# Kernel tuning notes

Hardware: AMD Instinct MI355X
Metric: run time of the kernel (lower is better)

The kernel has to match this reference:

```python
import math
import jax, jax.numpy as jnp
import numpy as np

TOP_K, NC, ALPHA, BETA, EPS = 10, 80, 0.5, 6.0, 1e-9
IMG, STRIDES = 640, (8, 16, 32)


def _ciou(box1, box2, eps=1e-7):
    # box1: gt [bs,n,1,4], box2: pred [bs,1,na,4] -> [bs,n,na,1]
    b1x1, b1y1, b1x2, b1y2 = jnp.split(box1, 4, axis=-1)
    b2x1, b2y1, b2x2, b2y2 = jnp.split(box2, 4, axis=-1)
    w1, h1 = b1x2 - b1x1, b1y2 - b1y1 + eps
    w2, h2 = b2x2 - b2x1, b2y2 - b2y1 + eps
    inter = jnp.clip(jnp.minimum(b1x2, b2x2) - jnp.maximum(b1x1, b2x1), 0.0) * \
            jnp.clip(jnp.minimum(b1y2, b2y2) - jnp.maximum(b1y1, b2y1), 0.0)
    union = w1 * h1 + w2 * h2 - inter + eps
    iou = inter / union
    cw = jnp.maximum(b1x2, b2x2) - jnp.minimum(b1x1, b2x1)
    ch = jnp.maximum(b1y2, b2y2) - jnp.minimum(b1y1, b2y1)
    c2 = cw ** 2 + ch ** 2 + eps
    rho2 = ((b2x1 + b2x2 - b1x1 - b1x2) ** 2 + (b2y1 + b2y2 - b1y1 - b1y2) ** 2) / 4.0
    v = (4.0 / math.pi ** 2) * (jnp.arctan(w2 / h2) - jnp.arctan(w1 / h1)) ** 2
    alpha = jax.lax.stop_gradient(v / (v - iou + (1.0 + eps)))
    return iou - (rho2 / c2 + v * alpha)


def _assign(score, p_box, anchors, gt_labels, gt_box, mask):
    bs, na, nc = score.shape
    n = gt_box.shape[1]
    labels = gt_labels[..., 0].astype(jnp.int32)      # [bs,n]
    valid = mask > 0                                  # [bs,n,1] valid-gt mask
    # --- candidate mask: anchor center strictly inside gt box ---
    lt, rb = gt_box[..., :2], gt_box[..., 2:]
    d = jnp.concatenate([anchors[None, None] - lt[:, :, None],
                         rb[:, :, None] - anchors[None, None]], -1)  # [bs,n,na,4]
    mask_in_gts = d.min(-1) > 1e-9                    # [bs,n,na]
    mask_gts = mask_in_gts & valid
    # --- per-(gt,anchor) class score and CIoU overlap ---
    gathered = score[jnp.arange(bs)[:, None], :, labels]          # [bs,n,na]
    bbox_scores = jnp.where(mask_gts, gathered, 0.0)
    ov = _ciou(gt_box[:, :, None], p_box[:, None])[..., 0]        # [bs,n,na]
    overlaps = jnp.where(mask_gts, jnp.clip(ov, 0.0), 0.0)
    metric = jnp.where(mask_gts,
                       jnp.where(mask_gts, gathered, 1.0) ** ALPHA * overlaps ** BETA,
                       0.0)
    # --- top-k candidates per gt; suppress duplicated indices ---
    _, top_id = jax.lax.top_k(metric, TOP_K)          # [bs,n,TOP_K]
    top_id = jnp.where(valid, top_id, 0)
    bi = jnp.arange(bs)[:, None, None]
    ni = jnp.arange(n)[None, :, None]
    count = jnp.zeros((bs, n, na), jnp.int32).at[bi, ni, top_id].add(1)
    count = jnp.where(count > 1, 0, count)
    mask_pos = count.astype(metric.dtype) * mask_in_gts.astype(metric.dtype) * mask  # [bs,n,na]
    fg = mask_pos.sum(1)                              # [bs,na]
    # --- resolve anchors claimed by multiple gts via max overlap ---
    max_over = (jnp.arange(n)[None, :, None] == jnp.argmax(overlaps, 1)[:, None, :]).astype(metric.dtype)
    mask_pos = jnp.where(fg[:, None, :] > 1, max_over, mask_pos)
    fg = mask_pos.sum(1)
    # --- gather targets ---
    gt_idx = jnp.argmax(mask_pos, 1)                  # [bs,na]
    target_labels = jnp.clip(jnp.take_along_axis(labels, gt_idx, 1), 0)
    target_bboxes = jnp.take_along_axis(gt_box, gt_idx[..., None], 1)  # [bs,na,4]
    ts = jax.nn.one_hot(target_labels, NC, dtype=metric.dtype)
    ts = jnp.where(fg[..., None] > 0, ts, 0.0)
    # --- task-aligned score normalization ---
    metric = metric * mask_pos
    pos_metrics = metric.max(-1, keepdims=True)
    pos_overlaps = (overlaps * mask_pos).max(-1, keepdims=True)
    norm_metric = metric * pos_overlaps / (pos_metrics + EPS)
    target_scores = ts * norm_metric.max(1)[..., None]               # [bs,na,NC]
    return target_bboxes, target_scores, fg > 0


def setup_inputs() -> dict:
    key = jax.random.key(0)
    ks = jax.random.split(key, 8)
    bs, n_max = 16, 64
    # anchor points: grid cell centers for strides 8/16/32 at 640x640
    pts = []
    for s in STRIDES:
        g = IMG // s
        c = (jnp.arange(g, dtype=jnp.float32) + 0.5) * s
        gy, gx = jnp.meshgrid(c, c, indexing='ij')
        pts.append(jnp.stack([gx.ravel(), gy.ravel()], -1))
    anchors = jnp.concatenate(pts, 0)                 # [8400,2]
    na = anchors.shape[0]
    # predicted boxes centered near anchor points
    wh = jax.random.uniform(ks[0], (bs, na, 2), minval=8.0, maxval=128.0)
    ctr = anchors[None] + jax.random.normal(ks[1], (bs, na, 2)) * 4.0
    p_box = jnp.concatenate([ctr - wh / 2, ctr + wh / 2], -1)
    score = jax.random.uniform(ks[2], (bs, na, NC))
    # ground-truth boxes (valid x1<x2, y1<y2)
    gwh = jax.random.uniform(ks[3], (bs, n_max, 2), minval=16.0, maxval=256.0)
    gctr = jax.random.uniform(ks[4], (bs, n_max, 2), minval=0.0, maxval=float(IMG))
    gt_box = jnp.concatenate([gctr - gwh / 2, gctr + gwh / 2], -1)
    gt_labels = jax.random.randint(ks[5], (bs, n_max, 1), 0, NC)
    nvalid = jax.random.randint(ks[6], (bs, 1), 8, n_max + 1)
    mask = (jnp.arange(n_max)[None, :] < nvalid).astype(jnp.float32)[..., None]
    return {"score": score, "p_box": p_box, "anchors": anchors,
            "gt_labels": gt_labels, "gt_box": gt_box, "mask": mask}


def reference(score, p_box, anchors, gt_labels, gt_box, mask):
    return _assign(score, p_box, anchors, gt_labels, gt_box, mask)
```

## Files before the change

### kernel.cpp

```cpp
#include <hip/hip_runtime.h>
#include <math.h>

#define BS   16
#define NMAX 64
#define NA   8400
#define NCLS 80
#define TOPK 10
#define ROWS (BS * NMAX)
#define TOTAL (BS * NA)

typedef unsigned long long u64;

__device__ __forceinline__ float ciou_clip(
    float gx1, float gy1, float gx2, float gy2, float at1, float area1,
    float px1, float py1, float px2, float py2, float at2, float area2)
{
    float iw = fminf(gx2, px2) - fmaxf(gx1, px1);
    float ih = fminf(gy2, py2) - fmaxf(gy1, py1);
    float inter = fmaxf(iw, 0.f) * fmaxf(ih, 0.f);
    float uni = area1 + area2 - inter + 1e-7f;
    float iou = inter / uni;
    float cw = fmaxf(gx2, px2) - fminf(gx1, px1);
    float ch = fmaxf(gy2, py2) - fminf(gy1, py1);
    float c2 = cw * cw + ch * ch + 1e-7f;
    float dx = px1 + px2 - gx1 - gx2;
    float dy = py1 + py2 - gy1 - gy2;
    float rho2 = (dx * dx + dy * dy) * 0.25f;
    float dat = at2 - at1;
    float v = (4.0f / (float)(M_PI * M_PI)) * dat * dat;
    float alpha = v / (v - iou + (1.0f + 1e-7f));
    return fmaxf(iou - (rho2 / c2 + v * alpha), 0.f);
}

#define INS10(kk)                                                         \
    if ((kk) > L[9]) {                                                    \
        L[9] = (kk);                                                      \
        _Pragma("unroll")                                                 \
        for (int q = 9; q >= 1; q--)                                      \
            if (L[q] > L[q-1]) { u64 tt = L[q-1]; L[q-1] = L[q]; L[q] = tt; } \
    }

__global__ __launch_bounds__(128) void k1_rows(
    const float* __restrict__ score,
    const float* __restrict__ p_box,
    const int*   __restrict__ gt_labels,
    const float* __restrict__ gt_box,
    const float* __restrict__ mask,
    u64*   __restrict__ mask64,
    float* __restrict__ amt,
    float* __restrict__ aov)
{
    int row = blockIdx.x;
    if (mask[row] <= 0.f) return;
    int wid  = threadIdx.x >> 6;
    int lane = threadIdx.x & 63;
    int b = row >> 6, n = row & 63;

    float4 gb = ((const float4*)gt_box)[row];
    float w1 = gb.z - gb.x;
    float h1 = gb.w - gb.y + 1e-7f;
    float at1 = atanf(w1 / h1);
    float area1 = w1 * h1;
    int lbl = gt_labels[row];
    const float* sc = score + (size_t)b * NA * NCLS + lbl;
    const float4* pb = (const float4*)p_box + (size_t)b * NA;

    int ilo0 = max(0,  (int)floorf(gb.x * 0.125f   - 0.5f));
    int ihi0 = min(79, (int)ceilf (gb.z * 0.125f   - 0.5f));
    int jlo0 = max(0,  (int)floorf(gb.y * 0.125f   - 0.5f));
    int jhi0 = min(79, (int)ceilf (gb.w * 0.125f   - 0.5f));
    int ilo1 = max(0,  (int)floorf(gb.x * 0.0625f  - 0.5f));
    int ihi1 = min(39, (int)ceilf (gb.z * 0.0625f  - 0.5f));
    int jlo1 = max(0,  (int)floorf(gb.y * 0.0625f  - 0.5f));
    int jhi1 = min(39, (int)ceilf (gb.w * 0.0625f  - 0.5f));
    int ilo2 = max(0,  (int)floorf(gb.x * 0.03125f - 0.5f));
    int ihi2 = min(19, (int)ceilf (gb.z * 0.03125f - 0.5f));
    int jlo2 = max(0,  (int)floorf(gb.y * 0.03125f - 0.5f));
    int jhi2 = min(19, (int)ceilf (gb.w * 0.03125f - 0.5f));
    int nx0 = max(0, ihi0 - ilo0 + 1), ny0 = max(0, jhi0 - jlo0 + 1);
    int nx1 = max(0, ihi1 - ilo1 + 1), ny1 = max(0, jhi1 - jlo1 + 1);
    int nx2 = max(0, ihi2 - ilo2 + 1), ny2 = max(0, jhi2 - jlo2 + 1);
    int c0 = nx0 * ny0;
    int c1 = c0 + nx1 * ny1;
    int T  = c1 + nx2 * ny2;

    u64 L[10];
#pragma unroll
    for (int q = 0; q < 10; q++) L[q] = 0ull;

    for (int t = threadIdx.x; t < T; t += 128) {
        bool ge1 = t >= c0, ge2 = t >= c1;
        int local = t - (ge2 ? c1 : (ge1 ? c0 : 0));
        int nxl  = ge2 ? nx2  : (ge1 ? nx1  : nx0);
        int ilol = ge2 ? ilo2 : (ge1 ? ilo1 : ilo0);
        int jlol = ge2 ? jlo2 : (ge1 ? jlo1 : jlo0);
        int g    = ge2 ? 20   : (ge1 ? 40   : 80);
        int off  = ge2 ? 8000 : (ge1 ? 6400 : 0);
        float s  = ge2 ? 32.f : (ge1 ? 16.f : 8.f);
        int jj = local / nxl;
        int ii = local - jj * nxl;
        int i = ilol + ii, j = jlol + jj;
        int a = off + j * g + i;
        float ax = ((float)i + 0.5f) * s, ay = ((float)j + 0.5f) * s;
        float dmin = fminf(fminf(ax - gb.x, ay - gb.y),
                           fminf(gb.z - ax, gb.w - ay));
        if (dmin > 1e-9f) {
            float4 pv = pb[a];
            float w2 = pv.z - pv.x;
            float h2 = pv.w - pv.y + 1e-7f;
            float ov = ciou_clip(gb.x, gb.y, gb.z, gb.w, at1, area1,
                                 pv.x, pv.y, pv.z, pv.w,
                                 atanf(w2 / h2), w2 * h2);
            float o2 = ov * ov;
            float mt = sqrtf(sc[(size_t)a * NCLS]) * o2 * o2 * o2;
            u64 kk = ((u64)__float_as_uint(mt) << 32) | (unsigned)(~a);
            INS10(kk)
        }
    }
    if (wid == 0) {
        float ax = (float)lane * 8.f + 4.f, ay = 4.f;
        float dmin = fminf(fminf(ax - gb.x, ay - gb.y),
                           fminf(gb.z - ax, gb.w - ay));
        if (!(dmin > 1e-9f)) {
            u64 kk = (u64)(unsigned)(~lane);
            INS10(kk)
        }
    }

    __shared__ u64 skey[2 * TOPK];
    u64 wk = 0ull;
    for (int it = 0; it < TOPK; it++) {
        u64 m = L[0];
#pragma unroll
        for (int o = 1; o < 64; o <<= 1) {
            u64 v = __shfl_xor(m, o);
            if (v > m) m = v;
        }
        if (lane == it) wk = m;
        if (L[0] == m) {
#pragma unroll
            for (int q = 0; q < 9; q++) L[q] = L[q + 1];
            L[9] = 0ull;
        }
    }
    if (lane < TOPK) skey[wid * TOPK + lane] = wk;
    __syncthreads();

    if (wid == 0) {
        u64 ck = (lane < 2 * TOPK) ? skey[lane] : 0ull;
        u64 winkey = 0ull;
        for (int it = 0; it < TOPK; it++) {
            u64 m = ck;
#pragma unroll
            for (int o = 1; o < 64; o <<= 1) {
                u64 v = __shfl_xor(m, o);
                if (v > m) m = v;
            }
            if (lane == it) winkey = m;
            if (ck == m) ck = 0ull;
        }
        if (lane < TOPK && winkey) {
            int a = (int)(~(unsigned)(winkey & 0xffffffffu));
            float mt = __uint_as_float((unsigned)(winkey >> 32));
            bool l2a = a >= 8000, l1a = (a >= 6400) && !l2a;
            int loc = a - (l2a ? 8000 : (l1a ? 6400 : 0));
            int g   = l2a ? 20 : (l1a ? 40 : 80);
            float s = l2a ? 32.f : (l1a ? 16.f : 8.f);
            int j = loc / g, i = loc - j * g;
            float ax = ((float)i + 0.5f) * s, ay = ((float)j + 0.5f) * s;
            float dmin = fminf(fminf(ax - gb.x, ay - gb.y),
                               fminf(gb.z - ax, gb.w - ay));
            if (dmin > 1e-9f) {
                size_t idx = (size_t)b * NA + a;
                atomicOr(&mask64[idx], 1ull << n);
                float4 pv = pb[a];
                float w2 = pv.z - pv.x;
                float h2 = pv.w - pv.y + 1e-7f;
                float ov = ciou_clip(gb.x, gb.y, gb.z, gb.w, at1, area1,
                                     pv.x, pv.y, pv.z, pv.w,
                                     atanf(w2 / h2), w2 * h2);
                amt[idx] = mt;
                aov[idx] = ov;
            }
        }
    }
}

__global__ __launch_bounds__(256) void k3_resolve(
    const float* __restrict__ score,
    const float* __restrict__ p_box,
    const float* __restrict__ anchors,
    const int*   __restrict__ gt_labels,
    const float* __restrict__ gt_box,
    const float* __restrict__ mask,
    const u64*   __restrict__ mask64,
    const float* __restrict__ amt,
    const float* __restrict__ aov,
    int* __restrict__ gt_idx,
    unsigned char* __restrict__ fg_arr,
    float* __restrict__ tgt_mt,
    float* __restrict__ out_bbox,
    float* __restrict__ out_fg,
    float* __restrict__ pos_mt,
    float* __restrict__ pos_ov)
{
    int i = blockIdx.x * 256 + threadIdx.x;
    if (i >= TOTAL) return;
    int b = i / NA, a = i - b * NA;
    u64 bits = mask64[i];
    int fg0 = __popcll(bits);
    int gi = 0, fg = (fg0 > 0);
    float mt = 0.f, ov = 0.f;
    if (fg0 == 1) {
        gi = __ffsll(bits) - 1;
        mt = amt[i];
        ov = aov[i];
    } else if (fg0 > 1) {
        float2 axy = ((const float2*)anchors)[a];
        float4 pv = ((const float4*)p_box)[i];
        float w2 = pv.z - pv.x;
        float h2 = pv.w - pv.y + 1e-7f;
        float at2 = atanf(w2 / h2);
        float area2 = w2 * h2;
        const float* mrow = mask + b * NMAX;
        float best = -1.f; int argn = 0;
        for (int nn = 0; nn < NMAX; nn++) {
            float v = 0.f;
            if (mrow[nn] > 0.f) {
                int r = b * NMAX + nn;
                float4 gbv = ((const float4*)gt_box)[r];
                float dmin = fminf(fminf(axy.x - gbv.x, axy.y - gbv.y),
                                   fminf(gbv.z - axy.x, gbv.w - axy.y));
                if (dmin > 1e-9f) {
                    float w1 = gbv.z - gbv.x;
                    float h1 = gbv.w - gbv.y + 1e-7f;
                    v = ciou_clip(gbv.x, gbv.y, gbv.z, gbv.w,
                                  atanf(w1 / h1), w1 * h1,
                                  pv.x, pv.y, pv.z, pv.w, at2, area2);
                }
            }
            if (v > best) { best = v; argn = nn; }
        }
        gi = argn;
        ov = fmaxf(best, 0.f);
        int lbl = gt_labels[b * NMAX + argn]; if (lbl < 0) lbl = 0;
        float gath = score[((size_t)b * NA + a) * NCLS + lbl];
        float o2 = ov * ov;
        mt = sqrtf(gath) * o2 * o2 * o2;
    }
    int r = b * NMAX + gi;
    gt_idx[i] = gi;
    fg_arr[i] = (unsigned char)fg;
    tgt_mt[i] = mt;
    out_fg[i] = fg ? 1.f : 0.f;
    ((float4*)out_bbox)[i] = ((const float4*)gt_box)[r];
    if (fg) {
        atomicMax((int*)&pos_mt[r], __float_as_int(mt));
        atomicMax((int*)&pos_ov[r], __float_as_int(ov));
    }
}

__global__ __launch_bounds__(256) void k5_full(
    const int*   __restrict__ gt_idx,
    const unsigned char* __restrict__ fg_arr,
    const float* __restrict__ tgt_mt,
    const int*   __restrict__ gt_labels,
    const float* __restrict__ pos_mt,
    const float* __restrict__ pos_ov,
    float4* __restrict__ out_scores)
{
    int i = blockIdx.x * 256 + threadIdx.x;
    if (i >= TOTAL * (NCLS / 4)) return;
    int ba = i / (NCLS / 4);
    int c4 = (i - ba * (NCLS / 4)) * 4;
    float4 o = make_float4(0.f, 0.f, 0.f, 0.f);
    if (fg_arr[ba]) {
        int b = ba / NA;
        int r = b * NMAX + gt_idx[ba];
        int lbl = gt_labels[r]; if (lbl < 0) lbl = 0;
        if (lbl >= c4 && lbl < c4 + 4) {
            float val = tgt_mt[ba] * pos_ov[r] / (pos_mt[r] + 1e-9f);
            if (lbl == c4)     o.x = val;
            if (lbl == c4 + 1) o.y = val;
            if (lbl == c4 + 2) o.z = val;
            if (lbl == c4 + 3) o.w = val;
        }
    }
    out_scores[i] = o;
}

extern "C" void kernel_launch(void* const* d_in, const int* in_sizes, int n_in,
                              void* d_out, int out_size, void* d_ws, size_t ws_size,
                              hipStream_t stream) {
    (void)in_sizes; (void)n_in; (void)out_size; (void)ws_size;
    const float* score     = (const float*)d_in[0];
    const float* p_box     = (const float*)d_in[1];
    const float* anchors   = (const float*)d_in[2];
    const int*   gt_labels = (const int*)d_in[3];
    const float* gt_box    = (const float*)d_in[4];
    const float* mask      = (const float*)d_in[5];

    char* w = (char*)d_ws;
    u64*   mask64   = (u64*)w;                 w += (size_t)TOTAL * 8;
    float* pos_mt   = (float*)w;               w += (size_t)ROWS * 4;
    float* pos_ov   = (float*)w;               w += (size_t)ROWS * 4;
    float* amt      = (float*)w;               w += (size_t)TOTAL * 4;
    float* aov      = (float*)w;               w += (size_t)TOTAL * 4;
    int*   gt_idx   = (int*)w;                 w += (size_t)TOTAL * 4;
    float* tgt_mt   = (float*)w;               w += (size_t)TOTAL * 4;
    unsigned char* fg_arr = (unsigned char*)w; w += (size_t)TOTAL;

    float*  out_bbox   = (float*)d_out;
    float4* out_scores = (float4*)(out_bbox + (size_t)TOTAL * 4);
    float*  out_fg     = (float*)out_scores + (size_t)TOTAL * NCLS;

    hipMemsetAsync(mask64, 0, (size_t)TOTAL * 8 + (size_t)ROWS * 8, stream);

    hipLaunchKernelGGL(k1_rows, dim3(ROWS), dim3(128), 0, stream,
                       score, p_box, gt_labels, gt_box, mask,
                       mask64, amt, aov);
    hipLaunchKernelGGL(k3_resolve, dim3((TOTAL + 255) / 256), dim3(256), 0, stream,
                       score, p_box, anchors, gt_labels, gt_box, mask,
                       mask64, amt, aov,
                       gt_idx, fg_arr, tgt_mt, out_bbox, out_fg, pos_mt, pos_ov);
    hipLaunchKernelGGL(k5_full, dim3((TOTAL * (NCLS / 4) + 255) / 256), dim3(256), 0, stream,
                       gt_idx, fg_arr, tgt_mt, gt_labels, pos_mt, pos_ov,
                       (float4*)out_scores);
}
```

Measured before the change: 142.9 us.

## Replace dense per-anchor mask with compact top-k lists scanned in shared memory

The first kernel now writes each gt's top-k anchor indices, metrics and overlaps into a compact per-row list instead of atomically OR-ing into a dense per-anchor bitmask with scattered metric arrays. It also zeroes pos_mt/pos_ov itself, so the memset call goes away. The resolve kernel uses a 2D grid (anchors x batch), loads the batch's 640 candidate entries into shared memory, and has each thread scan them to rebuild its gt bitmask. This removes the memset and the dense scattered writes and atomics, at the cost of a 640-entry shared-memory scan per anchor thread.

```diff
diff --git a/kernel.cpp b/kernel.cpp
--- a/kernel.cpp
+++ b/kernel.cpp
@@ -8,6 +8,7 @@
 #define TOPK 10
 #define ROWS (BS * NMAX)
 #define TOTAL (BS * NA)
+#define NFIN (NMAX * TOPK)
 
 typedef unsigned long long u64;
 
@@ -46,15 +47,22 @@
     const int*   __restrict__ gt_labels,
     const float* __restrict__ gt_box,
     const float* __restrict__ mask,
-    u64*   __restrict__ mask64,
-    float* __restrict__ amt,
-    float* __restrict__ aov)
+    int*   __restrict__ fin_a,
+    float* __restrict__ fin_mt,
+    float* __restrict__ fin_ov,
+    float* __restrict__ pos_mt,
+    float* __restrict__ pos_ov)
 {
     int row = blockIdx.x;
-    if (mask[row] <= 0.f) return;
-    int wid  = threadIdx.x >> 6;
-    int lane = threadIdx.x & 63;
-    int b = row >> 6, n = row & 63;
+    int tid = threadIdx.x;
+    if (tid == 0) { pos_mt[row] = 0.f; pos_ov[row] = 0.f; }
+    if (mask[row] <= 0.f) {
+        if (tid < TOPK) fin_a[row * TOPK + tid] = -1;
+        return;
+    }
+    int wid  = tid >> 6;
+    int lane = tid & 63;
+    int b = row >> 6;
 
     float4 gb = ((const float4*)gt_box)[row];
     float w1 = gb.z - gb.x;
@@ -88,7 +96,7 @@
 #pragma unroll
     for (int q = 0; q < 10; q++) L[q] = 0ull;
 
-    for (int t = threadIdx.x; t < T; t += 128) {
+    for (int t = tid; t < T; t += 128) {
         bool ge1 = t >= c0, ge2 = t >= c1;
         int local = t - (ge2 ? c1 : (ge1 ? c0 : 0));
         int nxl  = ge2 ? nx2  : (ge1 ? nx1  : nx0);
@@ -159,29 +167,33 @@
             if (lane == it) winkey = m;
             if (ck == m) ck = 0ull;
         }
-        if (lane < TOPK && winkey) {
-            int a = (int)(~(unsigned)(winkey & 0xffffffffu));
-            float mt = __uint_as_float((unsigned)(winkey >> 32));
-            bool l2a = a >= 8000, l1a = (a >= 6400) && !l2a;
-            int loc = a - (l2a ? 8000 : (l1a ? 6400 : 0));
-            int g   = l2a ? 20 : (l1a ? 40 : 80);
-            float s = l2a ? 32.f : (l1a ? 16.f : 8.f);
-            int j = loc / g, i = loc - j * g;
-            float ax = ((float)i + 0.5f) * s, ay = ((float)j + 0.5f) * s;
-            float dmin = fminf(fminf(ax - gb.x, ay - gb.y),
-                               fminf(gb.z - ax, gb.w - ay));
-            if (dmin > 1e-9f) {
-                size_t idx = (size_t)b * NA + a;
-                atomicOr(&mask64[idx], 1ull << n);
-                float4 pv = pb[a];
-                float w2 = pv.z - pv.x;
-                float h2 = pv.w - pv.y + 1e-7f;
-                float ov = ciou_clip(gb.x, gb.y, gb.z, gb.w, at1, area1,
-                                     pv.x, pv.y, pv.z, pv.w,
-                                     atanf(w2 / h2), w2 * h2);
-                amt[idx] = mt;
-                aov[idx] = ov;
+        if (lane < TOPK) {
+            int slot = row * TOPK + lane;
+            int fa = -1;
+            if (winkey) {
+                int a = (int)(~(unsigned)(winkey & 0xffffffffu));
+                float mt = __uint_as_float((unsigned)(winkey >> 32));
+                bool l2a = a >= 8000, l1a = (a >= 6400) && !l2a;
+                int loc = a - (l2a ? 8000 : (l1a ? 6400 : 0));
+                int g   = l2a ? 20 : (l1a ? 40 : 80);
+                float s = l2a ? 32.f : (l1a ? 16.f : 8.f);
+                int j = loc / g, i = loc - j * g;
+                float ax = ((float)i + 0.5f) * s, ay = ((float)j + 0.5f) * s;
+                float dmin = fminf(fminf(ax - gb.x, ay - gb.y),
+                                   fminf(gb.z - ax, gb.w - ay));
+                if (dmin > 1e-9f) {
+                    fa = a;
+                    float4 pv = pb[a];
+                    float w2 = pv.z - pv.x;
+                    float h2 = pv.w - pv.y + 1e-7f;
+                    float ov = ciou_clip(gb.x, gb.y, gb.z, gb.w, at1, area1,
+                                         pv.x, pv.y, pv.z, pv.w,
+                                         atanf(w2 / h2), w2 * h2);
+                    fin_mt[slot] = mt;
+                    fin_ov[slot] = ov;
+                }
             }
+            fin_a[slot] = fa;
         }
     }
 }
@@ -193,9 +205,9 @@
     const int*   __restrict__ gt_labels,
     const float* __restrict__ gt_box,
     const float* __restrict__ mask,
-    const u64*   __restrict__ mask64,
-    const float* __restrict__ amt,
-    const float* __restrict__ aov,
+    const int*   __restrict__ fin_a,
+    const float* __restrict__ fin_mt,
+    const float* __restrict__ fin_ov,
     int* __restrict__ gt_idx,
     unsigned char* __restrict__ fg_arr,
     float* __restrict__ tgt_mt,
@@ -204,17 +216,37 @@
     float* __restrict__ pos_mt,
     float* __restrict__ pos_ov)
 {
-    int i = blockIdx.x * 256 + threadIdx.x;
-    if (i >= TOTAL) return;
-    int b = i / NA, a = i - b * NA;
-    u64 bits = mask64[i];
+    int b   = blockIdx.y;
+    int a   = blockIdx.x * 256 + threadIdx.x;
+
+    __shared__ int   s_fa[NFIN];
+    __shared__ float s_mt[NFIN];
+    __shared__ float s_ov[NFIN];
+    for (int e = threadIdx.x; e < NFIN; e += 256) {
+        s_fa[e] = fin_a[b * NFIN + e];
+        s_mt[e] = fin_mt[b * NFIN + e];
+        s_ov[e] = fin_ov[b * NFIN + e];
+    }
+    __syncthreads();
+    if (a >= NA) return;
+    int i = b * NA + a;
+
+    u64 bits = 0ull;
+    float mt = 0.f, ov = 0.f;
+    {
+        int e = 0;
+        for (int r = 0; r < NMAX; r++) {
+            u64 bit = 1ull << r;
+#pragma unroll
+            for (int s = 0; s < TOPK; s++, e++) {
+                if (s_fa[e] == a) { bits |= bit; mt = s_mt[e]; ov = s_ov[e]; }
+            }
+        }
+    }
     int fg0 = __popcll(bits);
     int gi = 0, fg = (fg0 > 0);
-    float mt = 0.f, ov = 0.f;
     if (fg0 == 1) {
         gi = __ffsll(bits) - 1;
-        mt = amt[i];
-        ov = aov[i];
     } else if (fg0 > 1) {
         float2 axy = ((const float2*)anchors)[a];
         float4 pv = ((const float4*)p_box)[i];
@@ -247,11 +279,13 @@
         float gath = score[((size_t)b * NA + a) * NCLS + lbl];
         float o2 = ov * ov;
         mt = sqrtf(gath) * o2 * o2 * o2;
+    } else {
+        mt = 0.f; ov = 0.f;
     }
     int r = b * NMAX + gi;
     gt_idx[i] = gi;
     fg_arr[i] = (unsigned char)fg;
-    tgt_mt[i] = mt;
+    tgt_mt[i] = fg ? mt : 0.f;
     out_fg[i] = fg ? 1.f : 0.f;
     ((float4*)out_bbox)[i] = ((const float4*)gt_box)[r];
     if (fg) {
@@ -301,11 +335,11 @@
     const float* mask      = (const float*)d_in[5];
 
     char* w = (char*)d_ws;
-    u64*   mask64   = (u64*)w;                 w += (size_t)TOTAL * 8;
+    int*   fin_a    = (int*)w;                 w += (size_t)ROWS * TOPK * 4;
+    float* fin_mt   = (float*)w;               w += (size_t)ROWS * TOPK * 4;
+    float* fin_ov   = (float*)w;               w += (size_t)ROWS * TOPK * 4;
     float* pos_mt   = (float*)w;               w += (size_t)ROWS * 4;
     float* pos_ov   = (float*)w;               w += (size_t)ROWS * 4;
-    float* amt      = (float*)w;               w += (size_t)TOTAL * 4;
-    float* aov      = (float*)w;               w += (size_t)TOTAL * 4;
     int*   gt_idx   = (int*)w;                 w += (size_t)TOTAL * 4;
     float* tgt_mt   = (float*)w;               w += (size_t)TOTAL * 4;
     unsigned char* fg_arr = (unsigned char*)w; w += (size_t)TOTAL;
@@ -314,14 +348,12 @@
     float4* out_scores = (float4*)(out_bbox + (size_t)TOTAL * 4);
     float*  out_fg     = (float*)out_scores + (size_t)TOTAL * NCLS;
 
-    hipMemsetAsync(mask64, 0, (size_t)TOTAL * 8 + (size_t)ROWS * 8, stream);
-
     hipLaunchKernelGGL(k1_rows, dim3(ROWS), dim3(128), 0, stream,
                        score, p_box, gt_labels, gt_box, mask,
-                       mask64, amt, aov);
-    hipLaunchKernelGGL(k3_resolve, dim3((TOTAL + 255) / 256), dim3(256), 0, stream,
+                       fin_a, fin_mt, fin_ov, pos_mt, pos_ov);
+    hipLaunchKernelGGL(k3_resolve, dim3((NA + 255) / 256, BS), dim3(256), 0, stream,
                        score, p_box, anchors, gt_labels, gt_box, mask,
-                       mask64, amt, aov,
+                       fin_a, fin_mt, fin_ov,
                        gt_idx, fg_arr, tgt_mt, out_bbox, out_fg, pos_mt, pos_ov);
     hipLaunchKernelGGL(k5_full, dim3((TOTAL * (NCLS / 4) + 255) / 256), dim3(256), 0, stream,
                        gt_idx, fg_arr, tgt_mt, gt_labels, pos_mt, pos_ov,
```

Result: slower. 170.0 us (+18.9%).
